# Performance work log

Hardware: AMD Instinct MI355X
Metric: run time of the kernel (lower is better)

The kernel has to match this reference:

```python
import jax, jax.numpy as jnp
import numpy as np
import math

STATE_DIM = 256
R_MIN, R_MAX = 0.4, 0.9
PHASE_MAX = 2.0 * math.pi
BATCH, SEQ = 8, 4096


def setup_inputs() -> dict:
    key = jax.random.key(0)
    k_x, k_u1, k_u2, k_br, k_bi, k_cr, k_ci = jax.random.split(key, 7)
    D = STATE_DIM
    x = jax.random.normal(k_x, (BATCH, SEQ, D), dtype=jnp.float32)
    # parameter init mirroring the torch module
    u1 = jax.random.uniform(k_u1, (D,), dtype=jnp.float32)
    nu_log = jnp.log(-0.5 * jnp.log(u1 * (R_MAX + R_MIN) * (R_MAX - R_MIN) + R_MIN ** 2))
    u2 = jax.random.uniform(k_u2, (D,), dtype=jnp.float32)
    theta_log = jnp.log(PHASE_MAX * u2)
    lam_mod = jnp.exp(-jnp.exp(nu_log))
    gamma_log = jnp.log(jnp.sqrt(1.0 - jnp.square(lam_mod)))
    s_b = 1.0 / math.sqrt(2 * D)
    s_c = 1.0 / math.sqrt(D)
    B_re = jax.random.normal(k_br, (D, D), dtype=jnp.float32) * s_b
    B_im = jax.random.normal(k_bi, (D, D), dtype=jnp.float32) * s_b
    C_re = jax.random.normal(k_cr, (D, D), dtype=jnp.float32) * s_c
    C_im = jax.random.normal(k_ci, (D, D), dtype=jnp.float32) * s_c
    return {"x": x, "nu_log": nu_log, "theta_log": theta_log, "gamma_log": gamma_log,
            "B_re": B_re, "B_im": B_im, "C_re": C_re, "C_im": C_im}


def _binop(e_i, e_j):
    # diagonal linear recurrence composition: (a, b) -> h_t = a*h_{t-1} + b
    a_i, b_i = e_i
    a_j, b_j = e_j
    return a_j * a_i, a_j * b_i + b_j


def reference(x, nu_log, theta_log, gamma_log, B_re, B_im, C_re, C_im):
    L_mod = jnp.exp(-jnp.exp(nu_log))                       # [D]
    theta = jnp.exp(theta_log)
    L_diag = (L_mod * jnp.cos(theta) + 1j * L_mod * jnp.sin(theta)).astype(jnp.complex64)
    B = (B_re + 1j * B_im).astype(jnpp.complex64) if False else (B_re + 1j * B_im).astype(jnp.complex64)
    C = (C_re + 1j * C_im).astype(jnp.complex64)
    B_norm = B * jnp.exp(gamma_log)[:, None]                # [D, D] complex
    # input projection: [B, T, D] @ B_norm.T -> complex [B, T, D]
    B_elems = x.astype(jnp.complex64) @ B_norm.T
    L_elems = jnp.broadcast_to(L_diag, B_elems.shape)       # [B, T, D]
    # parallel associative scan over time axis
    _, inner_states = jax.lax.associative_scan(_binop, (L_elems, B_elems), axis=1)
    return (inner_states @ C.T).real                        # [B, T, D] float32
```

## Files before the change

kernel.cpp:

```cpp
#include <hip/hip_runtime.h>
#include <math.h>

#define D 256
#define NBATCH 8
#define T 4096
#define M (NBATCH * T)
#define LC 64
#define NC (T / LC)

typedef __attribute__((ext_vector_type(8))) short bf16x8;
typedef __attribute__((ext_vector_type(4))) float f32x4;

__device__ __forceinline__ unsigned short f2bf(float f) {
    unsigned int u = __float_as_uint(f);
    u += 0x7fff + ((u >> 16) & 1);
    return (unsigned short)(u >> 16);
}
__device__ __forceinline__ float bf2f(unsigned short s) {
    return __uint_as_float(((unsigned int)s) << 16);
}

__device__ __forceinline__ void gl_lds16(const unsigned short* g, unsigned short* l) {
    __builtin_amdgcn_global_load_lds(
        (const __attribute__((address_space(1))) unsigned int*)g,
        (__attribute__((address_space(3))) unsigned int*)l, 16, 0, 0);
}

__global__ __launch_bounds__(256) void prep_all(const float* __restrict__ Bre,
                                                const float* __restrict__ Bim,
                                                const float* __restrict__ gamma_log,
                                                const float* __restrict__ Cre,
                                                const float* __restrict__ Cim,
                                                const float* __restrict__ nu_log,
                                                const float* __restrict__ theta_log,
                                                unsigned short* __restrict__ W2,
                                                unsigned short* __restrict__ W3i,
                                                float* __restrict__ Lr,
                                                float* __restrict__ Li) {
    int n = blockIdx.x, k = threadIdx.x;
    if (n < 512) {
        int r = n & 255;
        float g = expf(gamma_log[r]);
        const float* src = (n < 256) ? Bre : Bim;
        W2[(size_t)n * 256 + k] = f2bf(src[(size_t)r * 256 + k] * g);
    } else if (n < 768) {
        int r = n - 512;
        W3i[(size_t)r * 512 + 2 * k]     = f2bf(Cre[(size_t)r * 256 + k]);
        W3i[(size_t)r * 512 + 2 * k + 1] = f2bf(-Cim[(size_t)r * 256 + k]);
    } else {
        float lmod = expf(-expf(nu_log[k]));
        float th = expf(theta_log[k]);
        Lr[k] = lmod * cosf(th);
        Li[k] = lmod * sinf(th);
    }
}

__global__ __launch_bounds__(512) void proj_gemm(const float* __restrict__ x,
                                                 const unsigned short* __restrict__ W,
                                                 unsigned short* __restrict__ U4,
                                                 unsigned short* __restrict__ V4) {
    __shared__ __align__(16) unsigned short As[128 * 32];
    __shared__ __align__(16) unsigned short Bs[256 * 32];
    const int tid  = threadIdx.x;
    const int lane = tid & 63;
    const int wid  = tid >> 6;
    const int m0 = blockIdx.x * 128;
    const int n0 = blockIdx.y * 256;
    const int wr = wid >> 2, wc = wid & 3;

    f32x4 acc[4][4];
#pragma unroll
    for (int i = 0; i < 4; ++i)
#pragma unroll
        for (int j = 0; j < 4; ++j) acc[i][j] = (f32x4){0.f, 0.f, 0.f, 0.f};

    const int aq = tid & 7, arow = tid >> 3;
    const float* gx = x + (size_t)(m0 + arow) * 256 + aq * 4;
    unsigned short* lA = As + arow * 32 + aq * 4;
    const int sr = lane >> 2, sc = (lane & 3) * 8;
    const unsigned short* gW0 = W + (size_t)(n0 + wid * 32 + sr) * 256 + sc;
    const unsigned short* gW1 = gW0 + (size_t)16 * 256;
    unsigned short* lB0 = Bs + wid * 1024;
    unsigned short* lB1 = lB0 + 512;

    const int ar = lane & 15;
    const int ak = (lane >> 4) * 8;

    for (int k0 = 0; k0 < 256; k0 += 32) {
        gl_lds16(gW0 + k0, lB0);
        gl_lds16(gW1 + k0, lB1);
#pragma unroll
        for (int i = 0; i < 2; ++i) {
            float4 v = *(const float4*)(gx + (size_t)(64 * i) * 256 + k0);
            union { ushort4 s; unsigned long long u; } o;
            o.s.x = f2bf(v.x); o.s.y = f2bf(v.y); o.s.z = f2bf(v.z); o.s.w = f2bf(v.w);
            *(unsigned long long*)(lA + (size_t)i * 64 * 32) = o.u;
        }
        __syncthreads();
        bf16x8 a[4], b[4];
#pragma unroll
        for (int mi = 0; mi < 4; ++mi)
            a[mi] = *(const bf16x8*)(As + (wr * 64 + mi * 16 + ar) * 32 + ak);
#pragma unroll
        for (int ni = 0; ni < 4; ++ni)
            b[ni] = *(const bf16x8*)(Bs + (wc * 64 + ni * 16 + ar) * 32 + ak);
#pragma unroll
        for (int mi = 0; mi < 4; ++mi)
#pragma unroll
            for (int ni = 0; ni < 4; ++ni)
                acc[mi][ni] = __builtin_amdgcn_mfma_f32_16x16x32_bf16(a[mi], b[ni], acc[mi][ni], 0, 0, 0);
        __syncthreads();
    }

    const int crow = (lane >> 4) * 4;
    const int ccol = lane & 15;
    unsigned short* base = (n0 == 0) ? U4 : V4;
#pragma unroll
    for (int mi = 0; mi < 4; ++mi)
#pragma unroll
        for (int ni = 0; ni < 4; ++ni) {
            const int rg = (m0 + wr * 64 + mi * 16 + crow) >> 2;
            const int c = wc * 64 + ni * 16 + ccol;
            uint2 o;
            o.x = (unsigned int)f2bf(acc[mi][ni][0]) | ((unsigned int)f2bf(acc[mi][ni][1]) << 16);
            o.y = (unsigned int)f2bf(acc[mi][ni][2]) | ((unsigned int)f2bf(acc[mi][ni][3]) << 16);
            *(uint2*)(base + ((size_t)rg * 256 + c) * 4) = o;
        }
}

__global__ __launch_bounds__(512) void out_gemm(const unsigned short* __restrict__ A,
                                                const unsigned short* __restrict__ W,
                                                float* __restrict__ oF) {
    __shared__ __align__(16) unsigned short As[128 * 32];
    __shared__ __align__(16) unsigned short Bs[128 * 32];
    const int tid  = threadIdx.x;
    const int lane = tid & 63;
    const int wid  = tid >> 6;
    const int m0 = blockIdx.x * 128;
    const int n0 = blockIdx.y * 128;
    const int wr = wid >> 1, wc = wid & 1;

    f32x4 acc[2][4];
#pragma unroll
    for (int i = 0; i < 2; ++i)
#pragma unroll
        for (int j = 0; j < 4; ++j) acc[i][j] = (f32x4){0.f, 0.f, 0.f, 0.f};

    const int sr = lane >> 2;
    const int sc = (lane & 3) * 8;
    const unsigned short* gA0 = A + (size_t)(m0 + wid * 16 + sr) * 512 + sc;
    const unsigned short* gW0 = W + (size_t)(n0 + wid * 16 + sr) * 512 + sc;
    unsigned short* lA0 = As + wid * 512;
    unsigned short* lB0 = Bs + wid * 512;

    const int ar = lane & 15;
    const int ak = (lane >> 4) * 8;

    for (int k0 = 0; k0 < 512; k0 += 32) {
        gl_lds16(gA0 + k0, lA0);
        gl_lds16(gW0 + k0, lB0);
        __syncthreads();
        bf16x8 a[2], b[4];
#pragma unroll
        for (int mi = 0; mi < 2; ++mi)
            a[mi] = *(const bf16x8*)(As + (wr * 32 + mi * 16 + ar) * 32 + ak);
#pragma unroll
        for (int ni = 0; ni < 4; ++ni)
            b[ni] = *(const bf16x8*)(Bs + (wc * 64 + ni * 16 + ar) * 32 + ak);
#pragma unroll
        for (int mi = 0; mi < 2; ++mi)
#pragma unroll
            for (int ni = 0; ni < 4; ++ni)
                acc[mi][ni] = __builtin_amdgcn_mfma_f32_16x16x32_bf16(a[mi], b[ni], acc[mi][ni], 0, 0, 0);
        __syncthreads();
    }

    const int crow = (lane >> 4) * 4;
    const int ccol = lane & 15;
#pragma unroll
    for (int mi = 0; mi < 2; ++mi)
#pragma unroll
        for (int ni = 0; ni < 4; ++ni) {
            const int r = m0 + wr * 32 + mi * 16 + crow;
            const int c = n0 + wc * 64 + ni * 16 + ccol;
#pragma unroll
            for (int j = 0; j < 4; ++j)
                oF[(size_t)(r + j) * 256 + c] = acc[mi][ni][j];
        }
}

__global__ __launch_bounds__(256) void scan_ends(const unsigned short* __restrict__ U4,
                                                 const unsigned short* __restrict__ V4,
                                                 const float* __restrict__ Lr,
                                                 const float* __restrict__ Li,
                                                 float* __restrict__ cre, float* __restrict__ cim) {
    int d = threadIdx.x;
    int bc = blockIdx.x;
    float lr = Lr[d], li = Li[d];
    float hr = 0.f, hi = 0.f;
    for (int q = 0; q < 16; ++q) {
        size_t eidx = ((size_t)(bc * 16 + q) * 256 + d) * 4;
        uint2 uu = *(const uint2*)(U4 + eidx);
        uint2 vv = *(const uint2*)(V4 + eidx);
        unsigned int uw[2] = {uu.x, uu.y}, vw[2] = {vv.x, vv.y};
#pragma unroll
        for (int j = 0; j < 4; ++j) {
            float u = bf2f((unsigned short)(uw[j >> 1] >> ((j & 1) * 16)));
            float v = bf2f((unsigned short)(vw[j >> 1] >> ((j & 1) * 16)));
            float nr = fmaf(lr, hr, fmaf(-li, hi, u));
            float ni = fmaf(lr, hi, fmaf(li, hr, v));
            hr = nr; hi = ni;
        }
    }
    cre[(size_t)bc * 256 + d] = hr;
    cim[(size_t)bc * 256 + d] = hi;
}

__global__ __launch_bounds__(256) void scan_carry(float* __restrict__ cre, float* __restrict__ cim,
                                                  const float* __restrict__ Lr,
                                                  const float* __restrict__ Li) {
    int d = threadIdx.x;
    int b = blockIdx.x;
    float lr = Lr[d], li = Li[d];
    float ar = 1.f, ai = 0.f;
    for (int i = 0; i < LC; i++) {
        float nr = ar * lr - ai * li;
        float ni = ar * li + ai * lr;
        ar = nr; ai = ni;
    }
    float hr = 0.f, hi = 0.f;
    for (int c = 0; c < NC; c++) {
        size_t idx = ((size_t)b * NC + c) * 256 + d;
        float xr = cre[idx], xi = cim[idx];
        cre[idx] = hr;
        cim[idx] = hi;
        float nr = fmaf(ar, hr, fmaf(-ai, hi, xr));
        float ni = fmaf(ar, hi, fmaf(ai, hr, xi));
        hr = nr; hi = ni;
    }
}

__global__ __launch_bounds__(256) void scan_apply(const unsigned short* __restrict__ U4,
                                                  const unsigned short* __restrict__ V4,
                                                  const float* __restrict__ Lr,
                                                  const float* __restrict__ Li,
                                                  const float* __restrict__ cre,
                                                  const float* __restrict__ cim,
                                                  unsigned int* __restrict__ H32) {
    int d = threadIdx.x;
    int bc = blockIdx.x;
    float lr = Lr[d], li = Li[d];
    float hr = cre[(size_t)bc * 256 + d];
    float hi = cim[(size_t)bc * 256 + d];
    for (int q = 0; q < 16; ++q) {
        size_t eidx = ((size_t)(bc * 16 + q) * 256 + d) * 4;
        uint2 uu = *(const uint2*)(U4 + eidx);
        uint2 vv = *(const uint2*)(V4 + eidx);
        unsigned int uw[2] = {uu.x, uu.y}, vw[2] = {vv.x, vv.y};
#pragma unroll
        for (int j = 0; j < 4; ++j) {
            float u = bf2f((unsigned short)(uw[j >> 1] >> ((j & 1) * 16)));
            float v = bf2f((unsigned short)(vw[j >> 1] >> ((j & 1) * 16)));
            float nr = fmaf(lr, hr, fmaf(-li, hi, u));
            float ni = fmaf(lr, hi, fmaf(li, hr, v));
            hr = nr; hi = ni;
            H32[(size_t)(bc * 64 + q * 4 + j) * 256 + d] =
                (unsigned int)f2bf(hr) | ((unsigned int)f2bf(hi) << 16);
        }
    }
}

extern "C" void kernel_launch(void* const* d_in, const int* in_sizes, int n_in,
                              void* d_out, int out_size, void* d_ws, size_t ws_size,
                              hipStream_t stream) {
    const float* x         = (const float*)d_in[0];
    const float* nu_log    = (const float*)d_in[1];
    const float* theta_log = (const float*)d_in[2];
    const float* gamma_log = (const float*)d_in[3];
    const float* B_re      = (const float*)d_in[4];
    const float* B_im      = (const float*)d_in[5];
    const float* C_re      = (const float*)d_in[6];
    const float* C_im      = (const float*)d_in[7];
    float* out = (float*)d_out;

    unsigned short* U4 = (unsigned short*)d_ws;
    unsigned short* V4 = U4 + (size_t)M * 256;
    unsigned short* H  = V4 + (size_t)M * 256;
    unsigned short* W2 = H + (size_t)M * 512;
    unsigned short* W3i = W2 + (size_t)512 * 256;
    float* cre = (float*)(W3i + (size_t)256 * 512);
    float* cim = cre + (size_t)NBATCH * NC * 256;
    float* Lr  = cim + (size_t)NBATCH * NC * 256;
    float* Li  = Lr + 256;

    prep_all<<<769, 256, 0, stream>>>(B_re, B_im, gamma_log, C_re, C_im,
                                      nu_log, theta_log, W2, W3i, Lr, Li);
    proj_gemm<<<dim3(M / 128, 2), 512, 0, stream>>>(x, W2, U4, V4);
    scan_ends<<<NBATCH * NC, 256, 0, stream>>>(U4, V4, Lr, Li, cre, cim);
    scan_carry<<<NBATCH, 256, 0, stream>>>(cre, cim, Lr, Li);
    scan_apply<<<NBATCH * NC, 256, 0, stream>>>(U4, V4, Lr, Li, cre, cim,
                                                (unsigned int*)H);
    out_gemm<<<dim3(M / 128, 2), 512, 0, stream>>>(H, W3i, out);
}
```

Before: 66.68 us.

## Cover full N per block in both GEMMs with 64-row M tiles

Both projection GEMMs now use 64-row M tiles, and each block covers the whole output width (512 columns for the input projection, 256 for the output projection) instead of splitting N across two grid columns. Each x tile is therefore read from global memory and converted to bf16 once rather than twice, and each H tile is loaded once in the output GEMM. The trade-off is a larger weight tile staged in LDS per block, smaller per-wave A reuse, and a different accumulator shape and register footprint.

```diff
diff --git a/kernel.cpp b/kernel.cpp
--- a/kernel.cpp
+++ b/kernel.cpp
@@ -59,53 +59,117 @@
                                                  const unsigned short* __restrict__ W,
                                                  unsigned short* __restrict__ U4,
                                                  unsigned short* __restrict__ V4) {
-    __shared__ __align__(16) unsigned short As[128 * 32];
+    __shared__ __align__(16) unsigned short As[64 * 32];
+    __shared__ __align__(16) unsigned short Bs[512 * 32];
+    const int tid  = threadIdx.x;
+    const int lane = tid & 63;
+    const int wid  = tid >> 6;
+    const int m0 = blockIdx.x * 64;
+    const int wr = wid >> 2, wc = wid & 3;
+
+    f32x4 acc[2][8];
+#pragma unroll
+    for (int i = 0; i < 2; ++i)
+#pragma unroll
+        for (int j = 0; j < 8; ++j) acc[i][j] = (f32x4){0.f, 0.f, 0.f, 0.f};
+
+    const int aq = tid & 7, arow = tid >> 3;
+    const float* gx = x + (size_t)(m0 + arow) * 256 + aq * 4;
+    unsigned short* lA = As + arow * 32 + aq * 4;
+    const int sr = lane >> 2, sc = (lane & 3) * 8;
+    const unsigned short* gW = W + (size_t)(wid * 64 + sr) * 256 + sc;
+    unsigned short* lB = Bs + wid * 2048;
+
+    const int ar = lane & 15;
+    const int ak = (lane >> 4) * 8;
+
+    for (int k0 = 0; k0 < 256; k0 += 32) {
+        gl_lds16(gW + k0,                    lB);
+        gl_lds16(gW + (size_t)16 * 256 + k0, lB + 512);
+        gl_lds16(gW + (size_t)32 * 256 + k0, lB + 1024);
+        gl_lds16(gW + (size_t)48 * 256 + k0, lB + 1536);
+        {
+            float4 v = *(const float4*)(gx + k0);
+            union { ushort4 s; unsigned long long u; } o;
+            o.s.x = f2bf(v.x); o.s.y = f2bf(v.y); o.s.z = f2bf(v.z); o.s.w = f2bf(v.w);
+            *(unsigned long long*)lA = o.u;
+        }
+        __syncthreads();
+        bf16x8 a[2], b[8];
+#pragma unroll
+        for (int mi = 0; mi < 2; ++mi)
+            a[mi] = *(const bf16x8*)(As + (wr * 32 + mi * 16 + ar) * 32 + ak);
+#pragma unroll
+        for (int ni = 0; ni < 8; ++ni)
+            b[ni] = *(const bf16x8*)(Bs + (wc * 128 + ni * 16 + ar) * 32 + ak);
+#pragma unroll
+        for (int mi = 0; mi < 2; ++mi)
+#pragma unroll
+            for (int ni = 0; ni < 8; ++ni)
+                acc[mi][ni] = __builtin_amdgcn_mfma_f32_16x16x32_bf16(a[mi], b[ni], acc[mi][ni], 0, 0, 0);
+        __syncthreads();
+    }
+
+    const int crow = (lane >> 4) * 4;
+    const int ccol = lane & 15;
+    unsigned short* base = (wc < 2) ? U4 : V4;
+    const int cb = (wc & 1) * 128;
+#pragma unroll
+    for (int mi = 0; mi < 2; ++mi)
+#pragma unroll
+        for (int ni = 0; ni < 8; ++ni) {
+            const int rg = (m0 + wr * 32 + mi * 16 + crow) >> 2;
+            const int c = cb + ni * 16 + ccol;
+            uint2 o;
+            o.x = (unsigned int)f2bf(acc[mi][ni][0]) | ((unsigned int)f2bf(acc[mi][ni][1]) << 16);
+            o.y = (unsigned int)f2bf(acc[mi][ni][2]) | ((unsigned int)f2bf(acc[mi][ni][3]) << 16);
+            *(uint2*)(base + ((size_t)rg * 256 + c) * 4) = o;
+        }
+}
+
+__global__ __launch_bounds__(512) void out_gemm(const unsigned short* __restrict__ A,
+                                                const unsigned short* __restrict__ W,
+                                                float* __restrict__ oF) {
+    __shared__ __align__(16) unsigned short As[64 * 32];
     __shared__ __align__(16) unsigned short Bs[256 * 32];
     const int tid  = threadIdx.x;
     const int lane = tid & 63;
     const int wid  = tid >> 6;
-    const int m0 = blockIdx.x * 128;
-    const int n0 = blockIdx.y * 256;
+    const int m0 = blockIdx.x * 64;
     const int wr = wid >> 2, wc = wid & 3;
 
-    f32x4 acc[4][4];
-#pragma unroll
-    for (int i = 0; i < 4; ++i)
+    f32x4 acc[2][4];
+#pragma unroll
+    for (int i = 0; i < 2; ++i)
 #pragma unroll
         for (int j = 0; j < 4; ++j) acc[i][j] = (f32x4){0.f, 0.f, 0.f, 0.f};
 
-    const int aq = tid & 7, arow = tid >> 3;
-    const float* gx = x + (size_t)(m0 + arow) * 256 + aq * 4;
-    unsigned short* lA = As + arow * 32 + aq * 4;
-    const int sr = lane >> 2, sc = (lane & 3) * 8;
-    const unsigned short* gW0 = W + (size_t)(n0 + wid * 32 + sr) * 256 + sc;
-    const unsigned short* gW1 = gW0 + (size_t)16 * 256;
+    const int sr = lane >> 2;
+    const int sc = (lane & 3) * 8;
+    const unsigned short* gA = A + (size_t)(m0 + (wid & 3) * 16 + sr) * 512 + sc;
+    unsigned short* lA = As + (wid & 3) * 512;
+    const unsigned short* gW0 = W + (size_t)(wid * 32 + sr) * 512 + sc;
+    const unsigned short* gW1 = gW0 + (size_t)16 * 512;
     unsigned short* lB0 = Bs + wid * 1024;
     unsigned short* lB1 = lB0 + 512;
 
     const int ar = lane & 15;
     const int ak = (lane >> 4) * 8;
 
-    for (int k0 = 0; k0 < 256; k0 += 32) {
+    for (int k0 = 0; k0 < 512; k0 += 32) {
+        if (wid < 4) gl_lds16(gA + k0, lA);
         gl_lds16(gW0 + k0, lB0);
         gl_lds16(gW1 + k0, lB1);
-#pragma unroll
-        for (int i = 0; i < 2; ++i) {
-            float4 v = *(const float4*)(gx + (size_t)(64 * i) * 256 + k0);
-            union { ushort4 s; unsigned long long u; } o;
-            o.s.x = f2bf(v.x); o.s.y = f2bf(v.y); o.s.z = f2bf(v.z); o.s.w = f2bf(v.w);
-            *(unsigned long long*)(lA + (size_t)i * 64 * 32) = o.u;
-        }
         __syncthreads();
-        bf16x8 a[4], b[4];
-#pragma unroll
-        for (int mi = 0; mi < 4; ++mi)
-            a[mi] = *(const bf16x8*)(As + (wr * 64 + mi * 16 + ar) * 32 + ak);
+        bf16x8 a[2], b[4];
+#pragma unroll
+        for (int mi = 0; mi < 2; ++mi)
+            a[mi] = *(const bf16x8*)(As + (wr * 32 + mi * 16 + ar) * 32 + ak);
 #pragma unroll
         for (int ni = 0; ni < 4; ++ni)
             b[ni] = *(const bf16x8*)(Bs + (wc * 64 + ni * 16 + ar) * 32 + ak);
 #pragma unroll
-        for (int mi = 0; mi < 4; ++mi)
+        for (int mi = 0; mi < 2; ++mi)
 #pragma unroll
             for (int ni = 0; ni < 4; ++ni)
                 acc[mi][ni] = __builtin_amdgcn_mfma_f32_16x16x32_bf16(a[mi], b[ni], acc[mi][ni], 0, 0, 0);
@@ -114,75 +178,12 @@
 
     const int crow = (lane >> 4) * 4;
     const int ccol = lane & 15;
-    unsigned short* base = (n0 == 0) ? U4 : V4;
-#pragma unroll
-    for (int mi = 0; mi < 4; ++mi)
-#pragma unroll
-        for (int ni = 0; ni < 4; ++ni) {
-            const int rg = (m0 + wr * 64 + mi * 16 + crow) >> 2;
-            const int c = wc * 64 + ni * 16 + ccol;
-            uint2 o;
-            o.x = (unsigned int)f2bf(acc[mi][ni][0]) | ((unsigned int)f2bf(acc[mi][ni][1]) << 16);
-            o.y = (unsigned int)f2bf(acc[mi][ni][2]) | ((unsigned int)f2bf(acc[mi][ni][3]) << 16);
-            *(uint2*)(base + ((size_t)rg * 256 + c) * 4) = o;
-        }
-}
-
-__global__ __launch_bounds__(512) void out_gemm(const unsigned short* __restrict__ A,
-                                                const unsigned short* __restrict__ W,
-                                                float* __restrict__ oF) {
-    __shared__ __align__(16) unsigned short As[128 * 32];
-    __shared__ __align__(16) unsigned short Bs[128 * 32];
-    const int tid  = threadIdx.x;
-    const int lane = tid & 63;
-    const int wid  = tid >> 6;
-    const int m0 = blockIdx.x * 128;
-    const int n0 = blockIdx.y * 128;
-    const int wr = wid >> 1, wc = wid & 1;
-
-    f32x4 acc[2][4];
-#pragma unroll
-    for (int i = 0; i < 2; ++i)
-#pragma unroll
-        for (int j = 0; j < 4; ++j) acc[i][j] = (f32x4){0.f, 0.f, 0.f, 0.f};
-
-    const int sr = lane >> 2;
-    const int sc = (lane & 3) * 8;
-    const unsigned short* gA0 = A + (size_t)(m0 + wid * 16 + sr) * 512 + sc;
-    const unsigned short* gW0 = W + (size_t)(n0 + wid * 16 + sr) * 512 + sc;
-    unsigned short* lA0 = As + wid * 512;
-    unsigned short* lB0 = Bs + wid * 512;
-
-    const int ar = lane & 15;
-    const int ak = (lane >> 4) * 8;
-
-    for (int k0 = 0; k0 < 512; k0 += 32) {
-        gl_lds16(gA0 + k0, lA0);
-        gl_lds16(gW0 + k0, lB0);
-        __syncthreads();
-        bf16x8 a[2], b[4];
-#pragma unroll
-        for (int mi = 0; mi < 2; ++mi)
-            a[mi] = *(const bf16x8*)(As + (wr * 32 + mi * 16 + ar) * 32 + ak);
-#pragma unroll
-        for (int ni = 0; ni < 4; ++ni)
-            b[ni] = *(const bf16x8*)(Bs + (wc * 64 + ni * 16 + ar) * 32 + ak);
-#pragma unroll
-        for (int mi = 0; mi < 2; ++mi)
-#pragma unroll
-            for (int ni = 0; ni < 4; ++ni)
-                acc[mi][ni] = __builtin_amdgcn_mfma_f32_16x16x32_bf16(a[mi], b[ni], acc[mi][ni], 0, 0, 0);
-        __syncthreads();
-    }
-
-    const int crow = (lane >> 4) * 4;
-    const int ccol = lane & 15;
 #pragma unroll
     for (int mi = 0; mi < 2; ++mi)
 #pragma unroll
         for (int ni = 0; ni < 4; ++ni) {
             const int r = m0 + wr * 32 + mi * 16 + crow;
-            const int c = n0 + wc * 64 + ni * 16 + ccol;
+            const int c = wc * 64 + ni * 16 + ccol;
 #pragma unroll
             for (int j = 0; j < 4; ++j)
                 oF[(size_t)(r + j) * 256 + c] = acc[mi][ni][j];
@@ -295,10 +296,10 @@
 
     prep_all<<<769, 256, 0, stream>>>(B_re, B_im, gamma_log, C_re, C_im,
                                       nu_log, theta_log, W2, W3i, Lr, Li);
-    proj_gemm<<<dim3(M / 128, 2), 512, 0, stream>>>(x, W2, U4, V4);
+    proj_gemm<<<M / 64, 512, 0, stream>>>(x, W2, U4, V4);
     scan_ends<<<NBATCH * NC, 256, 0, stream>>>(U4, V4, Lr, Li, cre, cim);
     scan_carry<<<NBATCH, 256, 0, stream>>>(cre, cim, Lr, Li);
     scan_apply<<<NBATCH * NC, 256, 0, stream>>>(U4, V4, Lr, Li, cre, cim,
                                                 (unsigned int*)H);
-    out_gemm<<<dim3(M / 128, 2), 512, 0, stream>>>(H, W3i, out);
-}
+    out_gemm<<<M / 64, 512, 0, stream>>>(H, W3i, out);
+}
```

After: 77.87 us. 16.8% more time.
